# Kernel optimization log

Hardware: AMD Instinct MI355X
Metric: run time of the kernel (lower is better)

The kernel has to match this reference:

```python
import jax, jax.numpy as jnp
import numpy as np

COMMITMENT_COST = 0.25


def setup_inputs() -> dict:
    key = jax.random.key(0)
    k1, k2 = jax.random.split(key)
    B, K, D = 1048576, 16, 64
    z = jax.random.normal(k1, (B, D), dtype=jnp.float32)
    # nn.Embedding init: uniform(-1/K, 1/K)
    embedding = jax.random.uniform(k2, (K, D), dtype=jnp.float32,
                                   minval=-1.0 / K, maxval=1.0 / K)
    return {"z": z, "embedding": embedding}


def reference(z, embedding):
    # squared L2 distances: ||z||^2 + ||e||^2 - 2 z e^T  -> [B, K]
    distances = (jnp.sum(z * z, axis=1, keepdims=True)
                 + jnp.sum(embedding * embedding, axis=1)
                 - 2.0 * jnp.matmul(z, embedding.T))
    encoding_indices = jnp.argmin(distances, axis=1)           # [B]
    quantized = embedding[encoding_indices]                    # [B, D]

    commitment_loss = jnp.mean((z - jax.lax.stop_gradient(quantized)) ** 2)
    embedding_loss = jnp.mean((jax.lax.stop_gradient(z) - quantized) ** 2)
    vq_loss = embedding_loss + COMMITMENT_COST * commitment_loss

    # straight-through estimator
    quantized = z + jax.lax.stop_gradient(quantized - z)
    return quantized, encoding_indices, vq_loss
```

## Files before the change

kernel.cpp:

```cpp
#include <hip/hip_runtime.h>

#define B_ROWS 1048576
#define K_CODES 16
#define D_DIM 64

constexpr int BLOCK = 256;
constexpr int GRID  = 2048;

typedef float f32x4 __attribute__((ext_vector_type(4)));

__device__ __forceinline__ float xor1_dpp(float x) {
    return __builtin_bit_cast(float,
        __builtin_amdgcn_update_dpp(0, __builtin_bit_cast(int, x), 0xB1, 0xF, 0xF, true));
}
__device__ __forceinline__ float xor2_dpp(float x) {
    return __builtin_bit_cast(float,
        __builtin_amdgcn_update_dpp(0, __builtin_bit_cast(int, x), 0x4E, 0xF, 0xF, true));
}
__device__ __forceinline__ float xor7_dpp(float x) {
    return __builtin_bit_cast(float,
        __builtin_amdgcn_update_dpp(0, __builtin_bit_cast(int, x), 0x141, 0xF, 0xF, true));
}
__device__ __forceinline__ float xor15_dpp(float x) {
    return __builtin_bit_cast(float,
        __builtin_amdgcn_update_dpp(0, __builtin_bit_cast(int, x), 0x140, 0xF, 0xF, true));
}

__global__ __launch_bounds__(BLOCK, 4)
void vq_main(const float* __restrict__ z,
             const float* __restrict__ emb,
             float* __restrict__ out_q,
             float* __restrict__ out_idx,
             float* __restrict__ partials)
{
    __shared__ __align__(16) float s_emb[K_CODES * D_DIM];
    __shared__ float s_se[K_CODES];
    __shared__ float s_w[BLOCK / 64];

    const int t = threadIdx.x;

    ((float4*)s_emb)[t] = ((const float4*)emb)[t];
    __syncthreads();

    if (t < K_CODES) {
        float s = 0.f;
        #pragma unroll
        for (int c = 0; c < D_DIM; ++c) {
            float e = s_emb[t * D_DIM + c];
            s = fmaf(e, e, s);
        }
        s_se[t] = s;
    }
    __syncthreads();

    const int j = t & 15;
    const int sj = ((j & 1) ? 8 : 0) ^ ((j & 2) ? 4 : 0)
                 ^ ((j & 4) ? 14 : 0) ^ ((j & 8) ? 3 : 0);

    float4 ereg[16];
    #pragma unroll
    for (int r = 0; r < 16; ++r)
        ereg[r] = *(const float4*)&s_emb[((r ^ j) * D_DIM) + sj * 4];
    const float se_j = s_se[j];

    float lossacc = 0.f;

    const int gid    = (blockIdx.x * BLOCK + t) >> 4;
    const int stride = (GRID * BLOCK) >> 4;

    int row = gid;
    f32x4 zv  = __builtin_nontemporal_load((const f32x4*)&z[(size_t)row * D_DIM + sj * 4]);
    f32x4 zn1 = zv;
    if (row + stride < B_ROWS)
        zn1 = __builtin_nontemporal_load((const f32x4*)&z[(size_t)(row + stride) * D_DIM + sj * 4]);

    while (row < B_ROWS) {
        const int prow = row + 2 * stride;
        f32x4 zn2 = zv;
        if (prow < B_ROWS)
            zn2 = __builtin_nontemporal_load((const f32x4*)&z[(size_t)prow * D_DIM + sj * 4]);

        float p[16];
        #pragma unroll
        for (int r = 0; r < 16; ++r) {
            float4 e = ereg[r];
            p[r] = fmaf(zv.w, e.w, fmaf(zv.z, e.z, fmaf(zv.y, e.y, zv.x * e.x)));
        }

        float szp = fmaf(zv.w, zv.w, fmaf(zv.z, zv.z, fmaf(zv.y, zv.y, zv.x * zv.x)));
        szp += xor1_dpp(szp);
        szp += xor2_dpp(szp);
        szp += xor7_dpp(szp);
        szp += xor15_dpp(szp);

        #pragma unroll
        for (int r = 0; r < 8; ++r)  p[r] += xor15_dpp(p[15 - r]);
        #pragma unroll
        for (int r = 0; r < 4; ++r)  p[r] += xor7_dpp(p[7 - r]);
        p[0] += xor2_dpp(p[2]);
        p[1] += xor2_dpp(p[3]);
        p[0] += xor1_dpp(p[1]);
        const float dot = p[0];

        const float d = (szp + se_j) - 2.0f * dot;

        float vmin = d;
        vmin = fminf(vmin, xor1_dpp(vmin));
        vmin = fminf(vmin, xor2_dpp(vmin));
        vmin = fminf(vmin, xor7_dpp(vmin));
        vmin = fminf(vmin, xor15_dpp(vmin));
        unsigned long long bal = __ballot(d == vmin);
        unsigned int mask = (unsigned int)((bal >> (t & 48)) & 0xFFFFull);
        int kmin = __ffs(mask) - 1;

        const float4 qv = *(const float4*)&s_emb[kmin * D_DIM + sj * 4];

        float dx = zv.x - qv.x; lossacc = fmaf(dx, dx, lossacc);
        dx = zv.y - qv.y;       lossacc = fmaf(dx, dx, lossacc);
        dx = zv.z - qv.z;       lossacc = fmaf(dx, dx, lossacc);
        dx = zv.w - qv.w;       lossacc = fmaf(dx, dx, lossacc);

        f32x4 qn = { qv.x, qv.y, qv.z, qv.w };
        __builtin_nontemporal_store(qn, (f32x4*)&out_q[(size_t)row * D_DIM + sj * 4]);
        if (j == 0) out_idx[row] = (float)kmin;

        zv  = zn1;
        zn1 = zn2;
        row += stride;
    }

    lossacc += __shfl_xor(lossacc, 32, 64);
    lossacc += __shfl_xor(lossacc, 16, 64);
    lossacc += __shfl_xor(lossacc, 8, 64);
    lossacc += __shfl_xor(lossacc, 4, 64);
    lossacc += __shfl_xor(lossacc, 2, 64);
    lossacc += __shfl_xor(lossacc, 1, 64);
    if ((t & 63) == 0) s_w[t >> 6] = lossacc;
    __syncthreads();
    if (t == 0) partials[blockIdx.x] = (s_w[0] + s_w[1]) + (s_w[2] + s_w[3]);
}

__global__ void vq_finalize(const float* __restrict__ partials, int n,
                            float* __restrict__ out_loss)
{
    __shared__ float sw[4];
    float s = 0.f;
    for (int i = threadIdx.x; i < n; i += 256) s += partials[i];
    s += __shfl_xor(s, 32, 64);
    s += __shfl_xor(s, 16, 64);
    s += __shfl_xor(s, 8, 64);
    s += __shfl_xor(s, 4, 64);
    s += __shfl_xor(s, 2, 64);
    s += __shfl_xor(s, 1, 64);
    if ((threadIdx.x & 63) == 0) sw[threadIdx.x >> 6] = s;
    __syncthreads();
    if (threadIdx.x == 0) {
        float tot = (sw[0] + sw[1]) + (sw[2] + sw[3]);
        *out_loss = tot * (1.25f / (float)(B_ROWS * (size_t)D_DIM));
    }
}

extern "C" void kernel_launch(void* const* d_in, const int* in_sizes, int n_in,
                              void* d_out, int out_size, void* d_ws, size_t ws_size,
                              hipStream_t stream)
{
    const float* z   = (const float*)d_in[0];
    const float* emb = (const float*)d_in[1];
    float* out      = (float*)d_out;
    float* out_q    = out;
    float* out_idx  = out + (size_t)B_ROWS * D_DIM;
    float* out_loss = out_idx + B_ROWS;
    float* partials = (float*)d_ws;

    vq_main<<<GRID, BLOCK, 0, stream>>>(z, emb, out_q, out_idx, partials);
    vq_finalize<<<1, 256, 0, stream>>>(partials, GRID, out_loss);
}
```

Baseline: 100.9 us.

## Fuse loss finalize into main kernel via ticket and deepen z prefetch

Drops the separate finalize kernel: each block writes its partial loss, takes an atomic ticket, and the last block to finish reduces all partials and writes the loss. The row loop now runs a fixed 32 iterations with a three-deep prefetch of z rows instead of two. This removes one kernel launch and gives more loads in flight, but adds a memset on every call and relies on B being an exact multiple of the grid stride.

```diff
diff --git a/kernel.cpp b/kernel.cpp
--- a/kernel.cpp
+++ b/kernel.cpp
@@ -31,11 +31,14 @@
              const float* __restrict__ emb,
              float* __restrict__ out_q,
              float* __restrict__ out_idx,
-             float* __restrict__ partials)
+             float* __restrict__ out_loss,
+             float* __restrict__ partials,
+             unsigned int* __restrict__ ticket)
 {
     __shared__ __align__(16) float s_emb[K_CODES * D_DIM];
     __shared__ float s_se[K_CODES];
     __shared__ float s_w[BLOCK / 64];
+    __shared__ int s_last;
 
     const int t = threadIdx.x;
 
@@ -69,16 +72,17 @@
     const int stride = (GRID * BLOCK) >> 4;
 
     int row = gid;
-    f32x4 zv  = __builtin_nontemporal_load((const f32x4*)&z[(size_t)row * D_DIM + sj * 4]);
-    f32x4 zn1 = zv;
-    if (row + stride < B_ROWS)
-        zn1 = __builtin_nontemporal_load((const f32x4*)&z[(size_t)(row + stride) * D_DIM + sj * 4]);
+    f32x4 z0 = __builtin_nontemporal_load((const f32x4*)&z[(size_t)row * D_DIM + sj * 4]);
+    f32x4 z1 = __builtin_nontemporal_load((const f32x4*)&z[(size_t)(row + stride) * D_DIM + sj * 4]);
+    f32x4 z2 = __builtin_nontemporal_load((const f32x4*)&z[(size_t)(row + 2 * stride) * D_DIM + sj * 4]);
 
-    while (row < B_ROWS) {
-        const int prow = row + 2 * stride;
-        f32x4 zn2 = zv;
-        if (prow < B_ROWS)
-            zn2 = __builtin_nontemporal_load((const f32x4*)&z[(size_t)prow * D_DIM + sj * 4]);
+    #pragma unroll 1
+    for (int k = 0; k < 32; ++k) {
+        f32x4 z3 = z0;
+        if (k < 29)
+            z3 = __builtin_nontemporal_load((const f32x4*)&z[(size_t)(row + 3 * stride) * D_DIM + sj * 4]);
+
+        const f32x4 zv = z0;
 
         float p[16];
         #pragma unroll
@@ -124,8 +128,7 @@
         __builtin_nontemporal_store(qn, (f32x4*)&out_q[(size_t)row * D_DIM + sj * 4]);
         if (j == 0) out_idx[row] = (float)kmin;
 
-        zv  = zn1;
-        zn1 = zn2;
+        z0 = z1; z1 = z2; z2 = z3;
         row += stride;
     }
 
@@ -137,26 +140,30 @@
     lossacc += __shfl_xor(lossacc, 1, 64);
     if ((t & 63) == 0) s_w[t >> 6] = lossacc;
     __syncthreads();
-    if (t == 0) partials[blockIdx.x] = (s_w[0] + s_w[1]) + (s_w[2] + s_w[3]);
-}
 
-__global__ void vq_finalize(const float* __restrict__ partials, int n,
-                            float* __restrict__ out_loss)
-{
-    __shared__ float sw[4];
-    float s = 0.f;
-    for (int i = threadIdx.x; i < n; i += 256) s += partials[i];
-    s += __shfl_xor(s, 32, 64);
-    s += __shfl_xor(s, 16, 64);
-    s += __shfl_xor(s, 8, 64);
-    s += __shfl_xor(s, 4, 64);
-    s += __shfl_xor(s, 2, 64);
-    s += __shfl_xor(s, 1, 64);
-    if ((threadIdx.x & 63) == 0) sw[threadIdx.x >> 6] = s;
+    if (t == 0) {
+        partials[blockIdx.x] = (s_w[0] + s_w[1]) + (s_w[2] + s_w[3]);
+        __threadfence();
+        s_last = (atomicAdd(ticket, 1u) == (unsigned)(GRID - 1));
+    }
     __syncthreads();
-    if (threadIdx.x == 0) {
-        float tot = (sw[0] + sw[1]) + (sw[2] + sw[3]);
-        *out_loss = tot * (1.25f / (float)(B_ROWS * (size_t)D_DIM));
+    if (s_last) {
+        float s = 0.f;
+        for (int i = t; i < GRID; i += 256)
+            s += __hip_atomic_load(&partials[i], __ATOMIC_RELAXED, __HIP_MEMORY_SCOPE_AGENT);
+        s += __shfl_xor(s, 32, 64);
+        s += __shfl_xor(s, 16, 64);
+        s += __shfl_xor(s, 8, 64);
+        s += __shfl_xor(s, 4, 64);
+        s += __shfl_xor(s, 2, 64);
+        s += __shfl_xor(s, 1, 64);
+        __syncthreads();
+        if ((t & 63) == 0) s_w[t >> 6] = s;
+        __syncthreads();
+        if (t == 0) {
+            float tot = (s_w[0] + s_w[1]) + (s_w[2] + s_w[3]);
+            *out_loss = tot * (1.25f / (float)(B_ROWS * (size_t)D_DIM));
+        }
     }
 }
 
@@ -171,7 +178,8 @@
     float* out_idx  = out + (size_t)B_ROWS * D_DIM;
     float* out_loss = out_idx + B_ROWS;
     float* partials = (float*)d_ws;
+    unsigned int* ticket = (unsigned int*)(partials + GRID);
 
-    vq_main<<<GRID, BLOCK, 0, stream>>>(z, emb, out_q, out_idx, partials);
-    vq_finalize<<<1, 256, 0, stream>>>(partials, GRID, out_loss);
+    hipMemsetAsync(ticket, 0, sizeof(unsigned int), stream);
+    vq_main<<<GRID, BLOCK, 0, stream>>>(z, emb, out_q, out_idx, out_loss, partials, ticket);
 }
```

Result: slower. 175.1 us (+73.6%).
